# Kernel tuning notes

Hardware: AMD Instinct MI355X
Metric: run time of the kernel (lower is better)

Reference implementation:

```python
import jax, jax.numpy as jnp
import numpy as np
from jax import lax

MID = 64      # mid_size -> token seq len = MID*MID = 4096
DM = 64       # d_model = in_channels
DI = 128      # d_inner = expand * d_model
DS = 16       # d_state
DC = 4        # d_conv
DTR = 4       # dt_rank = ceil(DM/16)
EPS = 1e-5


def conv3x3(x, w):
    return lax.conv_general_dilated(x, w, (1, 1), ((1, 1), (1, 1)),
                                    dimension_numbers=('NCHW', 'OIHW', 'NCHW'))


def layernorm(x, w, b):
    mu = jnp.mean(x, -1, keepdims=True)
    var = jnp.mean((x - mu) ** 2, -1, keepdims=True)
    return (x - mu) * lax.rsqrt(var + EPS) * w + b


def bilinear(x, h, w):
    b, c = x.shape[:2]
    return jax.image.resize(x, (b, c, h, w), method='bilinear', antialias=False)


def mamba(tok, in_w, conv_w, conv_b, xproj_w, dt_w, dt_b, Alog, D, out_w):
    # tok: (b, L, DM)
    b, L, _ = tok.shape
    xz = tok @ in_w.T                                # (b, L, 2*DI)
    xc, z = jnp.split(xz, 2, axis=-1)
    # causal depthwise conv1d over sequence
    xcT = xc.transpose(0, 2, 1)                      # (b, DI, L)
    xconv = lax.conv_general_dilated(xcT, conv_w, (1,), ((DC - 1, 0),),
                                     dimension_numbers=('NCH', 'OIH', 'NCH'),
                                     feature_group_count=DI)
    xconv = xconv + conv_b[None, :, None]
    u = jax.nn.silu(xconv.transpose(0, 2, 1))        # (b, L, DI)
    x_dbl = u @ xproj_w.T                            # (b, L, DTR+2*DS)
    dt, B, C = jnp.split(x_dbl, [DTR, DTR + DS], axis=-1)
    dt = jax.nn.softplus(dt @ dt_w.T + dt_b)         # (b, L, DI)
    A = -jnp.exp(Alog)                               # (DI, DS)
    dA = jnp.exp(dt[..., None] * A)                  # (b, L, DI, DS)
    dBu = dt[..., None] * B[:, :, None, :] * u[..., None]

    def step(h, xs):
        a_t, bu_t = xs
        h = a_t * h + bu_t
        return h, h

    h0 = jnp.zeros((b, DI, DS), dt.dtype)
    _, hs = lax.scan(step, h0, (dA.transpose(1, 0, 2, 3), dBu.transpose(1, 0, 2, 3)))
    y = jnp.einsum('lbns,bls->bln', hs, C) + u * D   # (b, L, DI)
    y = y * jax.nn.silu(z)
    return y @ out_w.T                               # (b, L, DM)


def setup_inputs() -> dict:
    key = jax.random.key(0)
    ks = iter(jax.random.split(key, 32))
    s = 0.02
    d = {}
    d['x'] = jax.random.normal(next(ks), (4, 64, 128, 128), jnp.float32)
    for n, shp in [('cb_w1', (64, 64, 3, 3)), ('cb_w2', (64, 64, 3, 3)),
                   ('sm_w1', (64, 64, 3, 3)), ('sm_w2', (64, 64, 3, 3))]:
        d[n] = jax.random.normal(next(ks), shp, jnp.float32) * s
    d['ln1_w'] = jnp.ones((DM,), jnp.float32); d['ln1_b'] = jnp.zeros((DM,), jnp.float32)
    d['ln2_w'] = jnp.ones((DM,), jnp.float32); d['ln2_b'] = jnp.zeros((DM,), jnp.float32)
    for p in ['m1', 'm2']:
        d[p + '_in_w'] = jax.random.normal(next(ks), (2 * DI, DM), jnp.float32) * s
        d[p + '_conv_w'] = jax.random.normal(next(ks), (DI, 1, DC), jnp.float32) * s
        d[p + '_conv_b'] = jnp.zeros((DI,), jnp.float32)
        d[p + '_xproj_w'] = jax.random.normal(next(ks), (DTR + 2 * DS, DI), jnp.float32) * s
        d[p + '_dt_w'] = jax.random.normal(next(ks), (DI, DTR), jnp.float32) * s
        d[p + '_dt_b'] = jnp.full((DI,), -2.0, jnp.float32)
        d[p + '_Alog'] = jnp.broadcast_to(jnp.log(jnp.arange(1, DS + 1, dtype=jnp.float32)), (DI, DS)).copy()
        d[p + '_D'] = jnp.ones((DI,), jnp.float32)
        d[p + '_out_w'] = jax.random.normal(next(ks), (DM, DI), jnp.float32) * s
    return d


def reference(x, cb_w1, cb_w2, ln1_w, ln1_b, ln2_w, ln2_b,
              m1_in_w, m1_conv_w, m1_conv_b, m1_xproj_w, m1_dt_w, m1_dt_b, m1_Alog, m1_D, m1_out_w,
              m2_in_w, m2_conv_w, m2_conv_b, m2_xproj_w, m2_dt_w, m2_dt_b, m2_Alog, m2_D, m2_out_w,
              sm_w1, sm_w2):
    b, c, h, w = x.shape
    xr = conv3x3(jax.nn.relu(conv3x3(x, cb_w1)), cb_w2) + x
    x_small = xr if (h, w) == (MID, MID) else bilinear(xr, MID, MID)
    tokens = x_small.reshape(b, c, MID * MID).transpose(0, 2, 1)   # (b, L, c)
    main = mamba(layernorm(tokens, ln1_w, ln1_b),
                 m1_in_w, m1_conv_w, m1_conv_b, m1_xproj_w, m1_dt_w, m1_dt_b, m1_Alog, m1_D, m1_out_w)
    gate_feat = mamba(layernorm(tokens, ln2_w, ln2_b),
                      m2_in_w, m2_conv_w, m2_conv_b, m2_xproj_w, m2_dt_w, m2_dt_b, m2_Alog, m2_D, m2_out_w)
    gate = jax.nn.softmax(gate_feat, axis=1)                       # softmax over token dim
    tokens = tokens + gate * main
    feat = tokens.transpose(0, 2, 1).reshape(b, c, MID, MID)
    if (h, w) != (MID, MID):
        feat = bilinear(feat, h, w)
    return conv3x3(jax.nn.relu(conv3x3(feat, sm_w1)), sm_w2)
```

## Files before the change

kernel.cpp:

```cpp
#include <hip/hip_runtime.h>

typedef unsigned int u32;
typedef unsigned short u16;
typedef __attribute__((ext_vector_type(8))) short short8;
typedef __attribute__((ext_vector_type(4))) float f32x4;

__device__ __forceinline__ float sigmoidf_(float x){
  return 1.f / (1.f + __expf(-x));
}
__device__ __forceinline__ u16 f2bf(float f){
  union { float f; u32 i; } v; v.f = f;
  u32 r = v.i + 0x7fffu + ((v.i >> 16) & 1u);
  return (u16)(r >> 16);
}
__device__ __forceinline__ float bf2f(u32 u){
  union { float f; u32 i; } v; v.i = (u & 0xffffu) << 16; return v.f;
}
__device__ __forceinline__ float softplus_(float x){
  return fmaxf(x, 0.f) + __logf(1.f + __expf(-fabsf(x)));
}

__global__ void k_wswz2b(const float* __restrict__ wA, u16* __restrict__ WHA, u16* __restrict__ WLA,
                         const float* __restrict__ wB, u16* __restrict__ WHB, u16* __restrict__ WLB,
                         u16* __restrict__ BPH, u16* __restrict__ BPL){
  int gidx = blockIdx.x * 256 + threadIdx.x;
  if (gidx < 73728){
    int sel = gidx >= 36864;
    int idx = gidx - sel * 36864;
    const float* w = sel ? wB : wA;
    u16* WH = sel ? WHB : WHA;
    u16* WL = sel ? WLB : WLA;
    int j    = idx & 7;
    int lane = (idx >> 3) & 63;
    int nt   = (idx >> 9) & 3;
    int kc   = (idx >> 11) & 1;
    int t    = idx >> 12;
    int ic = kc * 32 + ((lane >> 4) & 3) * 8 + j;
    int oc = nt * 16 + (lane & 15);
    float v = w[(oc * 64 + ic) * 9 + t];
    u16 h = f2bf(v);
    u16 l = f2bf(v - bf2f(h));
    WH[idx] = h; WL[idx] = l;
  } else {
    int i = gidx - 73728;
    if (i >= 2064) return;
    int b = i / 516, p = i - b * 516;
    int y, x;
    if (p < 130){ y = 0; x = p; }
    else if (p < 260){ y = 129; x = p - 130; }
    else if (p < 388){ y = p - 260 + 1; x = 0; }
    else { y = p - 388 + 1; x = 129; }
    size_t o = (((size_t)b * 130 + y) * 130 + x) * 64;
    uint4 z = make_uint4(0, 0, 0, 0);
#pragma unroll
    for (int q = 0; q < 8; q++){
      *(uint4*)(BPH + o + q * 8) = z;
      *(uint4*)(BPL + o + q * 8) = z;
    }
  }
}

__global__ __launch_bounds__(256) void k_prep(const float* __restrict__ src,
                                              u16* __restrict__ PH, u16* __restrict__ PL){
  __shared__ float ld[64 * 129];
  int yp = blockIdx.x;
  int b  = blockIdx.y;
  int ys = yp - 1;
  int tid = threadIdx.x;
  if ((u32)ys < 128u){
    for (int i = tid; i < 8192; i += 256){
      int c = i >> 7, x = i & 127;
      ld[c * 129 + x] = src[((size_t)(b * 64 + c) * 128 + ys) * 128 + x];
    }
  }
  __syncthreads();
  for (int i = tid; i < 130 * 64; i += 256){
    int xp = i >> 6, c = i & 63;
    float v = 0.f;
    if ((u32)ys < 128u && (u32)(xp - 1) < 128u) v = ld[c * 129 + (xp - 1)];
    u16 h = f2bf(v);
    u16 l = f2bf(v - bf2f(h));
    size_t o = (((size_t)b * 130 + yp) * 130 + xp) * 64 + c;
    PH[o] = h; PL[o] = l;
  }
}

__global__ __launch_bounds__(256) void k_prepup(const float* __restrict__ FEAT,
                                                u16* __restrict__ PH, u16* __restrict__ PL){
  __shared__ float ld0[64 * 65], ld1[64 * 65];
  int yp = blockIdx.x;
  int b  = blockIdx.y;
  int ys = yp - 1;
  int tid = threadIdx.x;
  float wy = 0.f;
  if ((u32)ys < 128u){
    float ay = 0.5f * ys - 0.25f;
    int fy = (int)floorf(ay); wy = ay - fy;
    int y0s = fy < 0 ? 0 : fy, y1s = fy + 1 > 63 ? 63 : fy + 1;
    for (int i = tid; i < 1024; i += 256){
      int c = i >> 4, x4 = (i & 15) * 4;
      float4 a0 = *(const float4*)&FEAT[((size_t)(b * 64 + c) * 64 + y0s) * 64 + x4];
      float4 a1 = *(const float4*)&FEAT[((size_t)(b * 64 + c) * 64 + y1s) * 64 + x4];
      ld0[c * 65 + x4 + 0] = a0.x; ld0[c * 65 + x4 + 1] = a0.y;
      ld0[c * 65 + x4 + 2] = a0.z; ld0[c * 65 + x4 + 3] = a0.w;
      ld1[c * 65 + x4 + 0] = a1.x; ld1[c * 65 + x4 + 1] = a1.y;
      ld1[c * 65 + x4 + 2] = a1.z; ld1[c * 65 + x4 + 3] = a1.w;
    }
  }
  __syncthreads();
  for (int i = tid; i < 130 * 64; i += 256){
    int xp = i >> 6, c = i & 63;
    float v = 0.f;
    int xs = xp - 1;
    if ((u32)ys < 128u && (u32)xs < 128u){
      float ax = 0.5f * xs - 0.25f;
      int fx = (int)floorf(ax); float wx = ax - fx;
      int x0s = fx < 0 ? 0 : fx, x1s = fx + 1 > 63 ? 63 : fx + 1;
      float v0 = (1.f - wx) * ld0[c * 65 + x0s] + wx * ld0[c * 65 + x1s];
      float v1 = (1.f - wx) * ld1[c * 65 + x0s] + wx * ld1[c * 65 + x1s];
      v = (1.f - wy) * v0 + wy * v1;
    }
    u16 h = f2bf(v);
    u16 l = f2bf(v - bf2f(h));
    size_t o = (((size_t)b * 130 + yp) * 130 + xp) * 64 + c;
    PH[o] = h; PL[o] = l;
  }
}

__global__ __launch_bounds__(256) void k_convm(
    const u16* __restrict__ PH, const u16* __restrict__ PL,
    const u16* __restrict__ WH, const u16* __restrict__ WL,
    const float* __restrict__ resid,
    u16* __restrict__ OBH, u16* __restrict__ OBL,
    float* __restrict__ OUTF, float* __restrict__ T, float* __restrict__ NT,
    int mode)
{
  __shared__ __align__(16) u32 smem[17344];
  u16* Ah_s = (u16*)smem;
  u16* Al_s = Ah_s + 10368;
  int tid = threadIdx.x;
  int lane = tid & 63, w = tid >> 6;
  int quad = lane >> 4, lcol = lane & 15;
  int b = blockIdx.z, y0 = blockIdx.y * 16, x0 = blockIdx.x * 16;

  f32x4 acc[4][4];
#pragma unroll
  for (int mt = 0; mt < 4; mt++)
#pragma unroll
    for (int nt = 0; nt < 4; nt++)
      acc[mt][nt] = (f32x4){0.f, 0.f, 0.f, 0.f};

  for (int kc = 0; kc < 2; kc++){
    __syncthreads();
    for (int i = tid; i < 1296; i += 256){
      int q = i & 3;
      int rc = i >> 2;
      int r = rc / 18, c = rc - r * 18;
      size_t so = (((size_t)b * 130 + y0 + r) * 130 + (x0 + c)) * 64 + kc * 32 + q * 8;
      int de = rc * 32 + q * 8;
      *(uint4*)(Ah_s + de) = *(const uint4*)(PH + so);
      *(uint4*)(Al_s + de) = *(const uint4*)(PL + so);
    }
    __syncthreads();
#pragma unroll
    for (int t = 0; t < 9; t++){
      int dy = t / 3, dx = t - dy * 3;
      short8 bh[4], bl[4];
#pragma unroll
      for (int nt = 0; nt < 4; nt++){
        int o = ((t * 2 + kc) * 4 + nt) * 512 + lane * 8;
        bh[nt] = *(const short8*)(WH + o);
        bl[nt] = *(const short8*)(WL + o);
      }
      short8 ah[4], al[4];
#pragma unroll
      for (int mt = 0; mt < 4; mt++){
        int e = ((w * 4 + mt + dy) * 18 + (lcol + dx)) * 32 + quad * 8;
        ah[mt] = *(const short8*)(Ah_s + e);
        al[mt] = *(const short8*)(Al_s + e);
      }
#pragma unroll
      for (int mt = 0; mt < 4; mt++)
#pragma unroll
        for (int nt = 0; nt < 4; nt++){
          acc[mt][nt] = __builtin_amdgcn_mfma_f32_16x16x32_bf16(ah[mt], bh[nt], acc[mt][nt], 0, 0, 0);
          acc[mt][nt] = __builtin_amdgcn_mfma_f32_16x16x32_bf16(ah[mt], bl[nt], acc[mt][nt], 0, 0, 0);
          acc[mt][nt] = __builtin_amdgcn_mfma_f32_16x16x32_bf16(al[mt], bh[nt], acc[mt][nt], 0, 0, 0);
        }
    }
  }

  __syncthreads();
  if (mode == 0){
    u32* epi = smem;
#pragma unroll
    for (int mt = 0; mt < 4; mt++){
      int row = w * 4 + mt;
#pragma unroll
      for (int nt = 0; nt < 4; nt++){
#pragma unroll
        for (int reg = 0; reg < 4; reg++){
          float v = fmaxf(acc[mt][nt][reg], 0.f);
          u32 h = f2bf(v);
          u32 l = f2bf(v - bf2f(h));
          int ccol = quad * 4 + reg;
          int oc = nt * 16 + lcol;
          epi[(row * 16 + ccol) * 66 + oc] = h | (l << 16);
        }
      }
    }
    __syncthreads();
    for (int i = tid; i < 16384; i += 256){
      int px = i >> 6, oc = i & 63;
      int row = px >> 4, ccol = px & 15;
      u32 pk = epi[px * 66 + oc];
      size_t o = (((size_t)b * 130 + y0 + row + 1) * 130 + (x0 + ccol + 1)) * 64 + oc;
      OBH[o] = (u16)pk;
      OBL[o] = (u16)(pk >> 16);
    }
  } else {
    float* epi = (float*)smem;
#pragma unroll
    for (int mt = 0; mt < 4; mt++){
      int row = w * 4 + mt;
#pragma unroll
      for (int nt = 0; nt < 4; nt++){
#pragma unroll
        for (int reg = 0; reg < 4; reg++){
          int px = row * 16 + quad * 4 + reg;
          int oc = nt * 16 + lcol;
          epi[oc * 259 + px] = acc[mt][nt][reg];
        }
      }
    }
    __syncthreads();
    if (mode == 1){
      for (int i = tid; i < 16384; i += 256){
        int oc = i >> 8, px = i & 255;
        int row = px >> 4, c = px & 15;
        size_t o = (((size_t)b * 64 + oc) * 128 + y0 + row) * 128 + x0 + c;
        float v = epi[oc * 259 + px];
        if (resid) v += resid[o];
        OUTF[o] = v;
      }
    } else {
      for (int i = tid; i < 16384; i += 256){
        int oc = i >> 8, px = i & 255;
        int row = px >> 4, c = px & 15;
        size_t o = (((size_t)b * 64 + oc) * 128 + y0 + row) * 128 + x0 + c;
        epi[oc * 259 + px] += resid[o];
      }
      __syncthreads();
      float* redS  = (float*)smem + 16576;
      float* redQ  = redS + 320;
      float* stats = redQ + 320;
      int token = tid & 63, cg2 = tid >> 6;
      int tr = token >> 3, tc = token & 7;
      float av[16]; float s = 0.f, q = 0.f;
      int p0 = (2 * tr) * 16 + 2 * tc;
#pragma unroll
      for (int j = 0; j < 16; j++){
        int c = cg2 * 16 + ((j + tr) & 15);
        const float* ep = epi + c * 259;
        float v = 0.25f * (ep[p0] + ep[p0 + 1] + ep[p0 + 16] + ep[p0 + 17]);
        av[j] = v; s += v; q = fmaf(v, v, q);
      }
      redS[token * 5 + cg2] = s;
      redQ[token * 5 + cg2] = q;
      __syncthreads();
      if (tid < 64){
        float S = 0.f, Q = 0.f;
        for (int g = 0; g < 4; g++){ S += redS[tid * 5 + g]; Q += redQ[tid * 5 + g]; }
        float mu = S * (1.f / 64.f);
        float var = Q * (1.f / 64.f) - mu * mu;
        stats[tid * 2] = mu;
        stats[tid * 2 + 1] = rsqrtf(var + 1e-5f);
      }
      __syncthreads();
      float mu = stats[token * 2], inv = stats[token * 2 + 1];
      int l = (blockIdx.y * 8 + tr) * 64 + blockIdx.x * 8 + tc;
      size_t to = ((size_t)b * 4096 + l) * 64;
#pragma unroll
      for (int j = 0; j < 16; j++){
        int c = cg2 * 16 + ((j + tr) & 15);
        T[to + c] = av[j];
        NT[to + c] = (av[j] - mu) * inv;
      }
    }
  }
}

__global__ __launch_bounds__(256) void k_fold2(
    const float* __restrict__ Wa, const float* __restrict__ lnwa, const float* __restrict__ lnba,
    float* __restrict__ W2a, float* __restrict__ B2a,
    const float* __restrict__ Wb, const float* __restrict__ lnwb, const float* __restrict__ lnbb,
    float* __restrict__ W2b, float* __restrict__ B2b){
  int m = blockIdx.x;
  const float* W   = m ? Wb   : Wa;
  const float* lnw = m ? lnwb : lnwa;
  const float* lnb = m ? lnbb : lnba;
  float* W2 = m ? W2b : W2a;
  float* B2 = m ? B2b : B2a;
  __shared__ float gw[64], gb[64];
  int j = threadIdx.x;
  if (j < 64){ gw[j] = lnw[j]; gb[j] = lnb[j]; }
  __syncthreads();
  float bias = 0.f;
#pragma unroll
  for (int k4 = 0; k4 < 16; k4++){
    float4 wv = *(const float4*)&W[j * 64 + k4 * 4];
    W2[j * 64 + k4 * 4 + 0] = wv.x * gw[k4 * 4 + 0];
    W2[j * 64 + k4 * 4 + 1] = wv.y * gw[k4 * 4 + 1];
    W2[j * 64 + k4 * 4 + 2] = wv.z * gw[k4 * 4 + 2];
    W2[j * 64 + k4 * 4 + 3] = wv.w * gw[k4 * 4 + 3];
    bias = fmaf(wv.x, gb[k4 * 4 + 0], bias);
    bias = fmaf(wv.y, gb[k4 * 4 + 1], bias);
    bias = fmaf(wv.z, gb[k4 * 4 + 2], bias);
    bias = fmaf(wv.w, gb[k4 * 4 + 3], bias);
  }
  B2[j] = bias;
}

__global__ __launch_bounds__(256) void k_inprojdw(
    const float* __restrict__ NT,
    const float* __restrict__ W2a, const float* __restrict__ B2a,
    float* __restrict__ Ua, float* __restrict__ Za,
    const float* __restrict__ cwa, const float* __restrict__ cba,
    const float* __restrict__ W2b, const float* __restrict__ B2b,
    float* __restrict__ Ub, float* __restrict__ Zb,
    const float* __restrict__ cwb, const float* __restrict__ cbb)
{
  __shared__ float wL[64 * 68];
  __shared__ float xcs[67 * 68];
  int mz = blockIdx.z;
  const float* W2 = mz ? W2b : W2a;
  const float* B2 = mz ? B2b : B2a;
  float* U = mz ? Ub : Ua;
  float* Z  = mz ? Zb : Za;
  const float* cw = mz ? cwb : cwa;
  const float* cb = mz ? cbb : cba;
  int tid = threadIdx.x;
  int t0 = blockIdx.x * 64;
  int j0 = blockIdx.y * 64;
  for (int i = tid; i < 4096; i += 256){
    int jl = i >> 6, k = i & 63;
    wL[jl * 68 + k] = W2[(size_t)(j0 + jl) * 64 + k];
  }
  __syncthreads();
  int tq = tid >> 4, cg = tid & 15;
  const float* ntp = NT + (size_t)(t0 + tq * 4) * 64;
  float acc[4][4];
#pragma unroll
  for (int c = 0; c < 4; c++){
    float bias = B2[j0 + cg + c * 16];
#pragma unroll
    for (int t = 0; t < 4; t++) acc[t][c] = bias;
  }
#pragma unroll 4
  for (int k4 = 0; k4 < 16; k4++){
    float4 lv[4];
#pragma unroll
    for (int t = 0; t < 4; t++)
      lv[t] = *(const float4*)(ntp + t * 64 + k4 * 4);
    float4 wv[4];
#pragma unroll
    for (int c = 0; c < 4; c++)
      wv[c] = *(const float4*)&wL[(cg + c * 16) * 68 + k4 * 4];
#pragma unroll
    for (int t = 0; t < 4; t++)
#pragma unroll
      for (int c = 0; c < 4; c++){
        acc[t][c] = fmaf(lv[t].x, wv[c].x, acc[t][c]);
        acc[t][c] = fmaf(lv[t].y, wv[c].y, acc[t][c]);
        acc[t][c] = fmaf(lv[t].z, wv[c].z, acc[t][c]);
        acc[t][c] = fmaf(lv[t].w, wv[c].w, acc[t][c]);
      }
  }
  if (j0 < 128){
    int isStart = ((t0 & 4095) == 0);
    if (tid < 192){
      int e = tid >> 6, col = tid & 63;
      float v = 0.f;
      if (!isStart){
        const float* np = NT + (size_t)(t0 - 3 + e) * 64;
        float a2 = B2[j0 + col];
#pragma unroll 4
        for (int k = 0; k < 64; k += 4){
          float4 nv = *(const float4*)(np + k);
          float4 wv = *(const float4*)&wL[col * 68 + k];
          a2 = fmaf(nv.x, wv.x, fmaf(nv.y, wv.y, fmaf(nv.z, wv.z, fmaf(nv.w, wv.w, a2))));
        }
        v = a2;
      }
      xcs[e * 68 + col] = v;
    }
#pragma unroll
    for (int t = 0; t < 4; t++)
#pragma unroll
      for (int c = 0; c < 4; c++)
        xcs[(3 + tq * 4 + t) * 68 + cg + c * 16] = acc[t][c];
    __syncthreads();
#pragma unroll
    for (int c = 0; c < 4; c++){
      int lc = cg + c * 16;
      int ch = j0 + lc;
      float4 wv = *(const float4*)(cw + ch * 4);
      float bias = cb[ch];
#pragma unroll
      for (int t = 0; t < 4; t++){
        int row = 3 + tq * 4 + t;
        float a = bias;
        a = fmaf(wv.w, xcs[row * 68 + lc], a);
        a = fmaf(wv.z, xcs[(row - 1) * 68 + lc], a);
        a = fmaf(wv.y, xcs[(row - 2) * 68 + lc], a);
        a = fmaf(wv.x, xcs[(row - 3) * 68 + lc], a);
        size_t tg = t0 + tq * 4 + t;
        U[tg * 128 + ch] = a * sigmoidf_(a);
      }
    }
  } else {
#pragma unroll
    for (int t = 0; t < 4; t++){
      size_t tg = t0 + tq * 4 + t;
#pragma unroll
      for (int c = 0; c < 4; c++)
        Z[tg * 128 + (j0 - 128) + cg + c * 16] = acc[t][c];
    }
  }
}

__global__ __launch_bounds__(256) void k_xprojdt(
    const float* __restrict__ U0, const float* __restrict__ XW0, float* __restrict__ DBL0,
    const float* __restrict__ U1, const float* __restrict__ XW1, float* __restrict__ DBL1)
{
  __shared__ float xw[36 * 132];
  int bid = blockIdx.x;
  int m = bid >> 7, blk = bid & 127;
  const float* Up   = m ? U1   : U0;
  const float* XWp  = m ? XW1  : XW0;
  float* DBLp = m ? DBL1 : DBL0;
  int tid = threadIdx.x;
  for (int i = tid; i < 4608; i += 256)
    xw[(i >> 7) * 132 + (i & 127)] = XWp[i];
  __syncthreads();
  int slot = tid >> 2, jq = tid & 3;
  size_t tgA = (size_t)blk * 128 + slot;
  size_t tgB = tgA + 64;
  const float4* upA = (const float4*)(Up + tgA * 128);
  const float4* upB = (const float4*)(Up + tgB * 128);
  float accA[9], accB[9];
#pragma unroll
  for (int jj = 0; jj < 9; jj++){ accA[jj] = 0.f; accB[jj] = 0.f; }
  for (int k4 = 0; k4 < 32; k4++){
    float4 uA = upA[k4];
    float4 uB = upB[k4];
#pragma unroll
    for (int jj = 0; jj < 9; jj++){
      float4 w = *(const float4*)&xw[(jq * 9 + jj) * 132 + k4 * 4];
      accA[jj] = fmaf(w.x, uA.x, fmaf(w.y, uA.y, fmaf(w.z, uA.z, fmaf(w.w, uA.w, accA[jj]))));
      accB[jj] = fmaf(w.x, uB.x, fmaf(w.y, uB.y, fmaf(w.z, uB.z, fmaf(w.w, uB.w, accB[jj]))));
    }
  }
#pragma unroll
  for (int jj = 0; jj < 9; jj++){
    DBLp[tgA * 36 + jq * 9 + jj] = accA[jj];
    DBLp[tgB * 36 + jq * 9 + jj] = accB[jj];
  }
}

__global__ __launch_bounds__(256) void k_scanA(
    const float* __restrict__ DBL0, const float* __restrict__ U0, const float* __restrict__ AL0,
    const float* __restrict__ DTW0, const float* __restrict__ DTB0,
    const float* __restrict__ DBL1, const float* __restrict__ U1, const float* __restrict__ AL1,
    const float* __restrict__ DTW1, const float* __restrict__ DTB1,
    float* __restrict__ HF, float* __restrict__ AP)
{
  __shared__ float su[64 * 65], sB[16 * 68], sdtr[256];
  int bid = blockIdx.x;
  int cg = bid & 1;
  int c  = (bid >> 1) & 63;
  int b  = (bid >> 7) & 3;
  int m  = bid >> 9;
  const float* DBLp = m ? DBL1 : DBL0;
  const float* Up   = m ? U1   : U0;
  const float* ALp  = m ? AL1  : AL0;
  const float* DTWp = m ? DTW1 : DTW0;
  const float* DTBp = m ? DTB1 : DTB0;
  int tid = threadIdx.x;
  int lane = tid & 63, w = tid >> 6;
  int lcol = lane & 15, q = lane >> 4;
  int chL = w * 16 + lcol;
  int n = cg * 64 + chL;
  size_t base = (size_t)b * 4096 + c * 64;
  for (int i = tid; i < 4096; i += 256){
    int ch = i & 63, l = i >> 6;
    su[l * 65 + ch] = Up[(base + l) * 128 + cg * 64 + ch];
  }
  for (int i = tid; i < 1024; i += 256){
    int s = i & 15, l = i >> 4;
    sB[s * 68 + l] = DBLp[(base + l) * 36 + 4 + s];
  }
  {
    int l = tid >> 2, jj = tid & 3;
    sdtr[tid] = DBLp[(base + l) * 36 + jj];
  }
  const float LOG2E = 1.4426950408889634f;
  float A1[4];
#pragma unroll
  for (int j = 0; j < 4; j++) A1[j] = -__expf(ALp[n * 16 + q * 4 + j]) * LOG2E;
  float4 wdt = *(const float4*)(DTWp + n * 4);
  float bdt = DTBp[n];
  __syncthreads();
  float h[4] = {0.f, 0.f, 0.f, 0.f};
  float ap[4] = {1.f, 1.f, 1.f, 1.f};
#pragma unroll
  for (int l4 = 0; l4 < 16; l4++){
    float4 Bv[4];
#pragma unroll
    for (int j = 0; j < 4; j++) Bv[j] = *(const float4*)&sB[(q * 4 + j) * 68 + l4 * 4];
#pragma unroll
    for (int jj = 0; jj < 4; jj++){
      int l = l4 * 4 + jj;
      float4 d = *(const float4*)&sdtr[l * 4];
      float x = bdt;
      x = fmaf(wdt.x, d.x, x); x = fmaf(wdt.y, d.y, x);
      x = fmaf(wdt.z, d.z, x); x = fmaf(wdt.w, d.w, x);
      float dt = softplus_(x);
      float u  = su[l * 65 + chL];
      float dtu = dt * u;
#pragma unroll
      for (int j = 0; j < 4; j++){
        float a = exp2f(dt * A1[j]);
        h[j] = fmaf(a, h[j], dtu * (&Bv[j].x)[jj]);
        ap[j] *= a;
      }
    }
  }
  size_t o = ((size_t)((m * 4 + b) * 64 + c)) * 2048 + n * 16 + q * 4;
  *(float4*)&HF[o] = make_float4(h[0], h[1], h[2], h[3]);
  *(float4*)&AP[o] = make_float4(ap[0], ap[1], ap[2], ap[3]);
}

__global__ __launch_bounds__(64) void k_scanB(
    const float* __restrict__ HF, const float* __restrict__ AP, float* __restrict__ HIN)
{
  int r = blockIdx.x * 64 + threadIdx.x;
  int q = r >> 11;
  int p = r & 2047;
  size_t base = (size_t)q * 64 * 2048 + p;
  float h = 0.f;
  for (int c8 = 0; c8 < 8; c8++){
    float a[8], f[8];
#pragma unroll
    for (int j = 0; j < 8; j++){
      size_t o = base + (size_t)(c8 * 8 + j) * 2048;
      a[j] = AP[o]; f[j] = HF[o];
    }
#pragma unroll
    for (int j = 0; j < 8; j++){
      size_t o = base + (size_t)(c8 * 8 + j) * 2048;
      HIN[o] = h;
      h = fmaf(a[j], h, f[j]);
    }
  }
}

__global__ __launch_bounds__(256) void k_scanC(
    const float* __restrict__ DBL0, const float* __restrict__ U0, const float* __restrict__ AL0,
    const float* __restrict__ DTW0, const float* __restrict__ DTB0,
    const float* __restrict__ D0, float* __restrict__ Y0,
    const float* __restrict__ DBL1, const float* __restrict__ U1, const float* __restrict__ AL1,
    const float* __restrict__ DTW1, const float* __restrict__ DTB1,
    const float* __restrict__ D1, float* __restrict__ Y1,
    const float* __restrict__ HIN)
{
  __shared__ float su[64 * 65], sB[16 * 68], sC[16 * 68], sdtr[256];
  int bid = blockIdx.x;
  int cg = bid & 1;
  int c  = (bid >> 1) & 63;
  int b  = (bid >> 7) & 3;
  int m  = bid >> 9;
  const float* DBLp = m ? DBL1 : DBL0;
  const float* Up   = m ? U1   : U0;
  const float* ALp  = m ? AL1  : AL0;
  const float* DTWp = m ? DTW1 : DTW0;
  const float* DTBp = m ? DTB1 : DTB0;
  const float* Dp   = m ? D1   : D0;
  float*       Yp   = m ? Y1   : Y0;
  int tid = threadIdx.x;
  int lane = tid & 63, w = tid >> 6;
  int lcol = lane & 15, q = lane >> 4;
  int chL = w * 16 + lcol;
  int n = cg * 64 + chL;
  size_t base = (size_t)b * 4096 + c * 64;
  for (int i = tid; i < 4096; i += 256){
    int ch = i & 63, l = i >> 6;
    su[l * 65 + ch] = Up[(base + l) * 128 + cg * 64 + ch];
  }
  for (int i = tid; i < 1024; i += 256){
    int s = i & 15, l = i >> 4;
    size_t ob = (base + l) * 36;
    sB[s * 68 + l] = DBLp[ob + 4 + s];
    sC[s * 68 + l] = DBLp[ob + 20 + s];
  }
  {
    int l = tid >> 2, jj = tid & 3;
    sdtr[tid] = DBLp[(base + l) * 36 + jj];
  }
  const float LOG2E = 1.4426950408889634f;
  float A1[4];
#pragma unroll
  for (int j = 0; j < 4; j++) A1[j] = -__expf(ALp[n * 16 + q * 4 + j]) * LOG2E;
  float4 wdt = *(const float4*)(DTWp + n * 4);
  float bdt = DTBp[n];
  float Dn = Dp[n];
  float4 hv = *(const float4*)&HIN[((size_t)((m * 4 + b) * 64 + c)) * 2048 + n * 16 + q * 4];
  float h[4] = {hv.x, hv.y, hv.z, hv.w};
  __syncthreads();
#pragma unroll
  for (int l4 = 0; l4 < 16; l4++){
    float4 Bv[4], Cv[4];
#pragma unroll
    for (int j = 0; j < 4; j++){
      Bv[j] = *(const float4*)&sB[(q * 4 + j) * 68 + l4 * 4];
      Cv[j] = *(const float4*)&sC[(q * 4 + j) * 68 + l4 * 4];
    }
#pragma unroll
    for (int jj = 0; jj < 4; jj++){
      int l = l4 * 4 + jj;
      float4 d = *(const float4*)&sdtr[l * 4];
      float x = bdt;
      x = fmaf(wdt.x, d.x, x); x = fmaf(wdt.y, d.y, x);
      x = fmaf(wdt.z, d.z, x); x = fmaf(wdt.w, d.w, x);
      float dt = softplus_(x);
      float u  = su[l * 65 + chL];
      float dtu = dt * u;
      float p = 0.f;
#pragma unroll
      for (int j = 0; j < 4; j++){
        float a = exp2f(dt * A1[j]);
        h[j] = fmaf(a, h[j], dtu * (&Bv[j].x)[jj]);
        p = fmaf(h[j], (&Cv[j].x)[jj], p);
      }
      p += __shfl_xor(p, 16);
      p += __shfl_xor(p, 32);
      if (q == 0)
        Yp[(base + l) * 128 + n] = fmaf(u, Dn, p);
    }
  }
}

__global__ __launch_bounds__(256) void k_outproj(
    const float* __restrict__ Y0, const float* __restrict__ Zg0,
    const float* __restrict__ W0, float* __restrict__ OUT0,
    const float* __restrict__ Y1, const float* __restrict__ Zg1,
    const float* __restrict__ W1, float* __restrict__ OUT1)
{
  __shared__ float yl[16 * 128];
  __shared__ float wT[128 * 65];
  int m = blockIdx.y;
  const float* Y  = m ? Y1  : Y0;
  const float* Zg = m ? Zg1 : Zg0;
  const float* W  = m ? W1  : W0;
  float* OUT = m ? OUT1 : OUT0;
  int tid = threadIdx.x;
  size_t t0 = (size_t)blockIdx.x * 16;
  for (int i = tid; i < 2048; i += 256){
    float z = Zg[t0 * 128 + i];
    yl[i] = Y[t0 * 128 + i] * (z * sigmoidf_(z));
  }
  for (int i = tid; i < 8192; i += 256){
    int k = i & 127, j = i >> 7;
    wT[k * 65 + j] = W[j * 128 + k];
  }
  __syncthreads();
  int j = tid & 63;
  int tg = tid >> 6;
  float acc[4] = {0.f, 0.f, 0.f, 0.f};
  for (int k = 0; k < 128; k += 4){
    float w0 = wT[k * 65 + j], w1 = wT[(k+1) * 65 + j];
    float w2 = wT[(k+2) * 65 + j], w3 = wT[(k+3) * 65 + j];
#pragma unroll
    for (int t = 0; t < 4; t++){
      float4 yv = *(const float4*)&yl[(tg * 4 + t) * 128 + k];
      acc[t] = fmaf(w0, yv.x, fmaf(w1, yv.y, fmaf(w2, yv.z, fmaf(w3, yv.w, acc[t]))));
    }
  }
#pragma unroll
  for (int t = 0; t < 4; t++)
    OUT[(t0 + tg * 4 + t) * 64 + j] = acc[t];
}

__global__ void k_smA(const float* __restrict__ G, float* __restrict__ P){
  int bid = blockIdx.x;
  int b = bid >> 6, lc = bid & 63;
  int tid = threadIdx.x;
  int j = tid & 63, part = tid >> 6;
  size_t base = (size_t)b * 4096 + lc * 64;
  float mx = -3.4e38f;
  for (int i = 0; i < 16; i++){
    int l = part + i * 4;
    mx = fmaxf(mx, G[(base + l) * 64 + j]);
  }
  float sm = 0.f;
  for (int i = 0; i < 16; i++){
    int l = part + i * 4;
    sm += __expf(G[(base + l) * 64 + j] - mx);
  }
  __shared__ float sM[256], sS[256];
  sM[tid] = mx; sS[tid] = sm;
  __syncthreads();
  if (tid < 64){
    float M = sM[tid], S = sS[tid];
    for (int p = 1; p < 4; p++){
      float m2 = sM[p * 64 + tid], s2 = sS[p * 64 + tid];
      float Mn = fmaxf(M, m2);
      S = S * __expf(M - Mn) + s2 * __expf(m2 - Mn);
      M = Mn;
    }
    P[(bid * 64 + tid) * 2] = M;
    P[(bid * 64 + tid) * 2 + 1] = S;
  }
}

__global__ void k_smB(const float* __restrict__ P, float* __restrict__ F){
  int tid = threadIdx.x;
  int b = tid >> 6, j = tid & 63;
  float M = -3.4e38f, S = 0.f;
  for (int lc = 0; lc < 64; lc++){
    int idx = ((b * 64 + lc) * 64 + j) * 2;
    float m2 = P[idx], s2 = P[idx + 1];
    float Mn = fmaxf(M, m2);
    S = S * __expf(M - Mn) + s2 * __expf(m2 - Mn);
    M = Mn;
  }
  F[(b * 64 + j) * 2] = M;
  F[(b * 64 + j) * 2 + 1] = S;
}

__global__ void k_combine(const float* __restrict__ T, const float* __restrict__ MAIN,
                          const float* __restrict__ G, const float* __restrict__ F,
                          float* __restrict__ FEAT){
  int bid = blockIdx.x;
  int b = bid >> 6, row = bid & 63;
  int tid = threadIdx.x;
  int j = tid & 63, ls = tid >> 6;
  __shared__ float tile[64 * 65];
  float M = F[(b * 64 + j) * 2], invS = 1.f / F[(b * 64 + j) * 2 + 1];
  size_t lbase = (size_t)b * 4096 + row * 64;
  for (int i = 0; i < 16; i++){
    int col = ls + i * 4;
    size_t off = (lbase + col) * 64 + j;
    float g = __expf(G[off] - M) * invS;
    tile[col * 65 + j] = T[off] + g * MAIN[off];
  }
  __syncthreads();
  int colw = tid & 63, jr = tid >> 6;
  for (int jj = jr; jj < 64; jj += 4)
    FEAT[(((size_t)b * 64 + jj) * 64 + row) * 64 + colw] = tile[colw * 65 + jj];
}

extern "C" void kernel_launch(void* const* d_in, const int* in_sizes, int n_in,
                              void* d_out, int out_size, void* d_ws, size_t ws_size,
                              hipStream_t stream) {
  const size_t P1A = 0, P1B = 4326400;
  const size_t MB0 = 0, MB1 = 10027008;
  const size_t O_LN = 0, O_XC = 1048576, O_Z = 3145728, O_U = 5242880,
               O_DBL = 9437184;
  const size_t TOK = 20054016, OUT0 = 21102592, OUT1 = 22151168;
  const size_t FEAT = 23208448;
  const size_t P3A = 4194304, P3B = 8520704;
  const size_t WA_H = 19000000, WA_L = 19018432, WB_H = 19036864, WB_L = 19055296;
  const size_t PADN = 2163200;
  const size_t SMP = 0, SMF = 65536;
  const size_t W2_0 = 21102592, B2_0 = 21118976, W2_1 = 21119232, B2_1 = 21135616;
  const size_t TOTAL = 24257024;
  if (ws_size < TOTAL * 4) return;

  float* ws = (float*)d_ws;
  const float* X   = (const float*)d_in[0];
  const float* CB1 = (const float*)d_in[1];
  const float* CB2 = (const float*)d_in[2];
  const float* SW1 = (const float*)d_in[3];
  const float* SW2 = (const float*)d_in[4];
  const float* LNW[2] = { (const float*)d_in[5], (const float*)d_in[7] };
  const float* LNB[2] = { (const float*)d_in[6], (const float*)d_in[8] };
  const float *INW[2], *CW[2], *CBb[2], *XPW[2], *DTW[2], *DTB[2], *AL[2], *DD[2], *OW[2];
  for (int m = 0; m < 2; m++){
    int p = 9 + m * 9;
    INW[m] = (const float*)d_in[p + 0];
    CW[m]  = (const float*)d_in[p + 1];
    CBb[m] = (const float*)d_in[p + 2];
    XPW[m] = (const float*)d_in[p + 3];
    DTW[m] = (const float*)d_in[p + 4];
    DTB[m] = (const float*)d_in[p + 5];
    AL[m]  = (const float*)d_in[p + 6];
    DD[m]  = (const float*)d_in[p + 7];
    OW[m]  = (const float*)d_in[p + 8];
  }

  u16* wah = (u16*)(ws + WA_H); u16* wal = (u16*)(ws + WA_L);
  u16* wbh = (u16*)(ws + WB_H); u16* wbl = (u16*)(ws + WB_L);

  {
    u16* pah = (u16*)(ws + P1A); u16* pal = pah + PADN * 2;
    u16* pbh = (u16*)(ws + P1B); u16* pbl = pbh + PADN * 2;
    k_wswz2b<<<297, 256, 0, stream>>>(CB1, wah, wal, CB2, wbh, wbl, pbh, pbl);
    k_prep<<<dim3(130, 4), 256, 0, stream>>>(X, pah, pal);
    k_convm<<<dim3(8, 8, 4), 256, 0, stream>>>(pah, pal, wah, wal, nullptr,
                                               pbh, pbl, nullptr, nullptr, nullptr, 0);
    k_convm<<<dim3(8, 8, 4), 256, 0, stream>>>(pbh, pbl, wbh, wbl, X,
                                               nullptr, nullptr, nullptr,
                                               ws + TOK, ws + MB0 + O_LN, 2);
  }

  k_fold2<<<2, 256, 0, stream>>>(INW[0], LNW[0], LNB[0], ws + W2_0, ws + B2_0,
                                 INW[1], LNW[1], LNB[1], ws + W2_1, ws + B2_1);
  k_inprojdw<<<dim3(256, 4, 2), 256, 0, stream>>>(
      ws + MB0 + O_LN,
      ws + W2_0, ws + B2_0, ws + MB0 + O_U, ws + MB0 + O_Z, CW[0], CBb[0],
      ws + W2_1, ws + B2_1, ws + MB1 + O_U, ws + MB1 + O_Z, CW[1], CBb[1]);
  k_xprojdt<<<256, 256, 0, stream>>>(
      ws + MB0 + O_U, XPW[0], ws + MB0 + O_DBL,
      ws + MB1 + O_U, XPW[1], ws + MB1 + O_DBL);

  float* HF  = ws + MB0 + O_XC;
  float* AP  = ws + MB0 + O_XC + 1048576;
  float* HIN = ws + MB0 + O_LN;

  k_scanA<<<1024, 256, 0, stream>>>(
      ws + MB0 + O_DBL, ws + MB0 + O_U, AL[0], DTW[0], DTB[0],
      ws + MB1 + O_DBL, ws + MB1 + O_U, AL[1], DTW[1], DTB[1],
      HF, AP);
  k_scanB<<<256, 64, 0, stream>>>(HF, AP, HIN);
  k_scanC<<<1024, 256, 0, stream>>>(
      ws + MB0 + O_DBL, ws + MB0 + O_U, AL[0], DTW[0], DTB[0], DD[0], ws + MB0 + O_XC,
      ws + MB1 + O_DBL, ws + MB1 + O_U, AL[1], DTW[1], DTB[1], DD[1], ws + MB1 + O_XC,
      HIN);

  k_outproj<<<dim3(1024, 2), 256, 0, stream>>>(
      ws + MB0 + O_XC, ws + MB0 + O_Z, OW[0], ws + OUT0,
      ws + MB1 + O_XC, ws + MB1 + O_Z, OW[1], ws + OUT1);

  k_smA<<<256, 256, 0, stream>>>(ws + OUT1, ws + SMP);
  k_smB<<<1, 256, 0, stream>>>(ws + SMP, ws + SMF);
  k_combine<<<256, 256, 0, stream>>>(ws + TOK, ws + OUT0, ws + OUT1, ws + SMF, ws + FEAT);

  {
    u16* pah = (u16*)(ws + P3A); u16* pal = pah + PADN * 2;
    u16* pbh = (u16*)(ws + P3B); u16* pbl = pbh + PADN * 2;
    k_wswz2b<<<297, 256, 0, stream>>>(SW1, wah, wal, SW2, wbh, wbl, pbh, pbl);
    k_prepup<<<dim3(130, 4), 256, 0, stream>>>(ws + FEAT, pah, pal);
    k_convm<<<dim3(8, 8, 4), 256, 0, stream>>>(pah, pal, wah, wal, nullptr,
                                               pbh, pbl, nullptr, nullptr, nullptr, 0);
    k_convm<<<dim3(8, 8, 4), 256, 0, stream>>>(pbh, pbl, wbh, wbl, nullptr,
                                               nullptr, nullptr, (float*)d_out,
                                               nullptr, nullptr, 1);
  }
}
```

Measured before the change: 397.0 us.

## Restructure chunked selective scan to one channel per thread with 16 states

The chunked scan kernels now give each thread a whole channel with all 16 states in registers, replacing the 4-states-per-lane layout that needed cross-lane shuffles to reduce the C·h output. Chunks shrink from 64 to 32 tokens, which doubles the number of chunks the sequential combine kernel walks. u is read straight from global memory with a two-step register prefetch instead of being staged through shared memory, and only the dt/B/C rows are staged. Scratch buffers move to free workspace regions. In exchange it raises register pressure (16 h, 16 A, 16 ap per thread) and lengthens the serial carry pass.

```diff
diff --git a/kernel.cpp b/kernel.cpp
--- a/kernel.cpp
+++ b/kernel.cpp
@@ -468,77 +468,82 @@
   }
 }
 
-__global__ __launch_bounds__(256) void k_scanA(
+#define STEPA(s, Bel) { float a_ = exp2f(dt * A1[s]); h[s] = fmaf(a_, h[s], dtu * (Bel)); ap[s] *= a_; }
+#define STEPC(s, Bel, Cel) { float a_ = exp2f(dt * A1[s]); h[s] = fmaf(a_, h[s], dtu * (Bel)); p = fmaf(h[s], (Cel), p); }
+
+__global__ __launch_bounds__(128) void k_scanA(
     const float* __restrict__ DBL0, const float* __restrict__ U0, const float* __restrict__ AL0,
     const float* __restrict__ DTW0, const float* __restrict__ DTB0,
     const float* __restrict__ DBL1, const float* __restrict__ U1, const float* __restrict__ AL1,
     const float* __restrict__ DTW1, const float* __restrict__ DTB1,
     float* __restrict__ HF, float* __restrict__ AP)
 {
-  __shared__ float su[64 * 65], sB[16 * 68], sdtr[256];
+  __shared__ float sd[32 * 20];
   int bid = blockIdx.x;
-  int cg = bid & 1;
-  int c  = (bid >> 1) & 63;
-  int b  = (bid >> 7) & 3;
-  int m  = bid >> 9;
+  int c = bid & 127, b = (bid >> 7) & 3, m = bid >> 9;
   const float* DBLp = m ? DBL1 : DBL0;
   const float* Up   = m ? U1   : U0;
   const float* ALp  = m ? AL1  : AL0;
   const float* DTWp = m ? DTW1 : DTW0;
   const float* DTBp = m ? DTB1 : DTB0;
-  int tid = threadIdx.x;
-  int lane = tid & 63, w = tid >> 6;
-  int lcol = lane & 15, q = lane >> 4;
-  int chL = w * 16 + lcol;
-  int n = cg * 64 + chL;
-  size_t base = (size_t)b * 4096 + c * 64;
-  for (int i = tid; i < 4096; i += 256){
-    int ch = i & 63, l = i >> 6;
-    su[l * 65 + ch] = Up[(base + l) * 128 + cg * 64 + ch];
-  }
-  for (int i = tid; i < 1024; i += 256){
-    int s = i & 15, l = i >> 4;
-    sB[s * 68 + l] = DBLp[(base + l) * 36 + 4 + s];
-  }
+  int ch = threadIdx.x;
+  size_t base = (size_t)b * 4096 + c * 32;
+  for (int i = ch; i < 160; i += 128){
+    int l = i / 5, part = i - l * 5;
+    *(float4*)&sd[l * 20 + part * 4] = *(const float4*)&DBLp[(base + l) * 36 + part * 4];
+  }
+  const float LOG2E = 1.4426950408889634f;
+  float A1[16];
   {
-    int l = tid >> 2, jj = tid & 3;
-    sdtr[tid] = DBLp[(base + l) * 36 + jj];
-  }
-  const float LOG2E = 1.4426950408889634f;
-  float A1[4];
-#pragma unroll
-  for (int j = 0; j < 4; j++) A1[j] = -__expf(ALp[n * 16 + q * 4 + j]) * LOG2E;
-  float4 wdt = *(const float4*)(DTWp + n * 4);
-  float bdt = DTBp[n];
-  __syncthreads();
-  float h[4] = {0.f, 0.f, 0.f, 0.f};
-  float ap[4] = {1.f, 1.f, 1.f, 1.f};
-#pragma unroll
-  for (int l4 = 0; l4 < 16; l4++){
-    float4 Bv[4];
-#pragma unroll
-    for (int j = 0; j < 4; j++) Bv[j] = *(const float4*)&sB[(q * 4 + j) * 68 + l4 * 4];
-#pragma unroll
-    for (int jj = 0; jj < 4; jj++){
-      int l = l4 * 4 + jj;
-      float4 d = *(const float4*)&sdtr[l * 4];
-      float x = bdt;
-      x = fmaf(wdt.x, d.x, x); x = fmaf(wdt.y, d.y, x);
-      x = fmaf(wdt.z, d.z, x); x = fmaf(wdt.w, d.w, x);
-      float dt = softplus_(x);
-      float u  = su[l * 65 + chL];
-      float dtu = dt * u;
-#pragma unroll
-      for (int j = 0; j < 4; j++){
-        float a = exp2f(dt * A1[j]);
-        h[j] = fmaf(a, h[j], dtu * (&Bv[j].x)[jj]);
-        ap[j] *= a;
-      }
-    }
-  }
-  size_t o = ((size_t)((m * 4 + b) * 64 + c)) * 2048 + n * 16 + q * 4;
-  *(float4*)&HF[o] = make_float4(h[0], h[1], h[2], h[3]);
-  *(float4*)&AP[o] = make_float4(ap[0], ap[1], ap[2], ap[3]);
+    float4 a0 = *(const float4*)&ALp[ch * 16 + 0];
+    float4 a1 = *(const float4*)&ALp[ch * 16 + 4];
+    float4 a2 = *(const float4*)&ALp[ch * 16 + 8];
+    float4 a3 = *(const float4*)&ALp[ch * 16 + 12];
+    A1[0] = -__expf(a0.x) * LOG2E; A1[1] = -__expf(a0.y) * LOG2E;
+    A1[2] = -__expf(a0.z) * LOG2E; A1[3] = -__expf(a0.w) * LOG2E;
+    A1[4] = -__expf(a1.x) * LOG2E; A1[5] = -__expf(a1.y) * LOG2E;
+    A1[6] = -__expf(a1.z) * LOG2E; A1[7] = -__expf(a1.w) * LOG2E;
+    A1[8] = -__expf(a2.x) * LOG2E; A1[9] = -__expf(a2.y) * LOG2E;
+    A1[10] = -__expf(a2.z) * LOG2E; A1[11] = -__expf(a2.w) * LOG2E;
+    A1[12] = -__expf(a3.x) * LOG2E; A1[13] = -__expf(a3.y) * LOG2E;
+    A1[14] = -__expf(a3.z) * LOG2E; A1[15] = -__expf(a3.w) * LOG2E;
+  }
+  float4 wdt = *(const float4*)(DTWp + ch * 4);
+  float bdt = DTBp[ch];
+  float h[16], ap[16];
+#pragma unroll
+  for (int s = 0; s < 16; s++){ h[s] = 0.f; ap[s] = 1.f; }
+  float ucur = Up[base * 128 + ch];
+  float unx  = Up[(base + 1) * 128 + ch];
+  __syncthreads();
+#pragma unroll
+  for (int l = 0; l < 32; l++){
+    float u2 = (l < 30) ? Up[(base + l + 2) * 128 + ch] : 0.f;
+    float4 d = *(const float4*)&sd[l * 20];
+    float x = bdt;
+    x = fmaf(wdt.x, d.x, x); x = fmaf(wdt.y, d.y, x);
+    x = fmaf(wdt.z, d.z, x); x = fmaf(wdt.w, d.w, x);
+    float dt = softplus_(x);
+    float dtu = dt * ucur;
+    float4 B0 = *(const float4*)&sd[l * 20 + 4];
+    float4 B1 = *(const float4*)&sd[l * 20 + 8];
+    float4 B2 = *(const float4*)&sd[l * 20 + 12];
+    float4 B3 = *(const float4*)&sd[l * 20 + 16];
+    STEPA(0, B0.x) STEPA(1, B0.y) STEPA(2, B0.z) STEPA(3, B0.w)
+    STEPA(4, B1.x) STEPA(5, B1.y) STEPA(6, B1.z) STEPA(7, B1.w)
+    STEPA(8, B2.x) STEPA(9, B2.y) STEPA(10, B2.z) STEPA(11, B2.w)
+    STEPA(12, B3.x) STEPA(13, B3.y) STEPA(14, B3.z) STEPA(15, B3.w)
+    ucur = unx; unx = u2;
+  }
+  size_t o = ((size_t)((m * 4 + b) * 128 + c)) * 2048 + (size_t)ch * 16;
+  *(float4*)&HF[o + 0]  = make_float4(h[0], h[1], h[2], h[3]);
+  *(float4*)&HF[o + 4]  = make_float4(h[4], h[5], h[6], h[7]);
+  *(float4*)&HF[o + 8]  = make_float4(h[8], h[9], h[10], h[11]);
+  *(float4*)&HF[o + 12] = make_float4(h[12], h[13], h[14], h[15]);
+  *(float4*)&AP[o + 0]  = make_float4(ap[0], ap[1], ap[2], ap[3]);
+  *(float4*)&AP[o + 4]  = make_float4(ap[4], ap[5], ap[6], ap[7]);
+  *(float4*)&AP[o + 8]  = make_float4(ap[8], ap[9], ap[10], ap[11]);
+  *(float4*)&AP[o + 12] = make_float4(ap[12], ap[13], ap[14], ap[15]);
 }
 
 __global__ __launch_bounds__(64) void k_scanB(
@@ -547,9 +552,9 @@
   int r = blockIdx.x * 64 + threadIdx.x;
   int q = r >> 11;
   int p = r & 2047;
-  size_t base = (size_t)q * 64 * 2048 + p;
+  size_t base = (size_t)q * 128 * 2048 + p;
   float h = 0.f;
-  for (int c8 = 0; c8 < 8; c8++){
+  for (int c8 = 0; c8 < 16; c8++){
     float a[8], f[8];
 #pragma unroll
     for (int j = 0; j < 8; j++){
@@ -565,7 +570,7 @@
   }
 }
 
-__global__ __launch_bounds__(256) void k_scanC(
+__global__ __launch_bounds__(128) void k_scanC(
     const float* __restrict__ DBL0, const float* __restrict__ U0, const float* __restrict__ AL0,
     const float* __restrict__ DTW0, const float* __restrict__ DTB0,
     const float* __restrict__ D0, float* __restrict__ Y0,
@@ -574,12 +579,9 @@
     const float* __restrict__ D1, float* __restrict__ Y1,
     const float* __restrict__ HIN)
 {
-  __shared__ float su[64 * 65], sB[16 * 68], sC[16 * 68], sdtr[256];
+  __shared__ float sd[32 * 36];
   int bid = blockIdx.x;
-  int cg = bid & 1;
-  int c  = (bid >> 1) & 63;
-  int b  = (bid >> 7) & 3;
-  int m  = bid >> 9;
+  int c = bid & 127, b = (bid >> 7) & 3, m = bid >> 9;
   const float* DBLp = m ? DBL1 : DBL0;
   const float* Up   = m ? U1   : U0;
   const float* ALp  = m ? AL1  : AL0;
@@ -587,66 +589,70 @@
   const float* DTBp = m ? DTB1 : DTB0;
   const float* Dp   = m ? D1   : D0;
   float*       Yp   = m ? Y1   : Y0;
-  int tid = threadIdx.x;
-  int lane = tid & 63, w = tid >> 6;
-  int lcol = lane & 15, q = lane >> 4;
-  int chL = w * 16 + lcol;
-  int n = cg * 64 + chL;
-  size_t base = (size_t)b * 4096 + c * 64;
-  for (int i = tid; i < 4096; i += 256){
-    int ch = i & 63, l = i >> 6;
-    su[l * 65 + ch] = Up[(base + l) * 128 + cg * 64 + ch];
-  }
-  for (int i = tid; i < 1024; i += 256){
-    int s = i & 15, l = i >> 4;
-    size_t ob = (base + l) * 36;
-    sB[s * 68 + l] = DBLp[ob + 4 + s];
-    sC[s * 68 + l] = DBLp[ob + 20 + s];
-  }
+  int ch = threadIdx.x;
+  size_t base = (size_t)b * 4096 + c * 32;
+  for (int i = ch; i < 288; i += 128){
+    int l = i / 9, part = i - l * 9;
+    *(float4*)&sd[l * 36 + part * 4] = *(const float4*)&DBLp[(base + l) * 36 + part * 4];
+  }
+  const float LOG2E = 1.4426950408889634f;
+  float A1[16];
   {
-    int l = tid >> 2, jj = tid & 3;
-    sdtr[tid] = DBLp[(base + l) * 36 + jj];
-  }
-  const float LOG2E = 1.4426950408889634f;
-  float A1[4];
-#pragma unroll
-  for (int j = 0; j < 4; j++) A1[j] = -__expf(ALp[n * 16 + q * 4 + j]) * LOG2E;
-  float4 wdt = *(const float4*)(DTWp + n * 4);
-  float bdt = DTBp[n];
-  float Dn = Dp[n];
-  float4 hv = *(const float4*)&HIN[((size_t)((m * 4 + b) * 64 + c)) * 2048 + n * 16 + q * 4];
-  float h[4] = {hv.x, hv.y, hv.z, hv.w};
-  __syncthreads();
-#pragma unroll
-  for (int l4 = 0; l4 < 16; l4++){
-    float4 Bv[4], Cv[4];
-#pragma unroll
-    for (int j = 0; j < 4; j++){
-      Bv[j] = *(const float4*)&sB[(q * 4 + j) * 68 + l4 * 4];
-      Cv[j] = *(const float4*)&sC[(q * 4 + j) * 68 + l4 * 4];
-    }
-#pragma unroll
-    for (int jj = 0; jj < 4; jj++){
-      int l = l4 * 4 + jj;
-      float4 d = *(const float4*)&sdtr[l * 4];
-      float x = bdt;
-      x = fmaf(wdt.x, d.x, x); x = fmaf(wdt.y, d.y, x);
-      x = fmaf(wdt.z, d.z, x); x = fmaf(wdt.w, d.w, x);
-      float dt = softplus_(x);
-      float u  = su[l * 65 + chL];
-      float dtu = dt * u;
-      float p = 0.f;
-#pragma unroll
-      for (int j = 0; j < 4; j++){
-        float a = exp2f(dt * A1[j]);
-        h[j] = fmaf(a, h[j], dtu * (&Bv[j].x)[jj]);
-        p = fmaf(h[j], (&Cv[j].x)[jj], p);
-      }
-      p += __shfl_xor(p, 16);
-      p += __shfl_xor(p, 32);
-      if (q == 0)
-        Yp[(base + l) * 128 + n] = fmaf(u, Dn, p);
-    }
+    float4 a0 = *(const float4*)&ALp[ch * 16 + 0];
+    float4 a1 = *(const float4*)&ALp[ch * 16 + 4];
+    float4 a2 = *(const float4*)&ALp[ch * 16 + 8];
+    float4 a3 = *(const float4*)&ALp[ch * 16 + 12];
+    A1[0] = -__expf(a0.x) * LOG2E; A1[1] = -__expf(a0.y) * LOG2E;
+    A1[2] = -__expf(a0.z) * LOG2E; A1[3] = -__expf(a0.w) * LOG2E;
+    A1[4] = -__expf(a1.x) * LOG2E; A1[5] = -__expf(a1.y) * LOG2E;
+    A1[6] = -__expf(a1.z) * LOG2E; A1[7] = -__expf(a1.w) * LOG2E;
+    A1[8] = -__expf(a2.x) * LOG2E; A1[9] = -__expf(a2.y) * LOG2E;
+    A1[10] = -__expf(a2.z) * LOG2E; A1[11] = -__expf(a2.w) * LOG2E;
+    A1[12] = -__expf(a3.x) * LOG2E; A1[13] = -__expf(a3.y) * LOG2E;
+    A1[14] = -__expf(a3.z) * LOG2E; A1[15] = -__expf(a3.w) * LOG2E;
+  }
+  float4 wdt = *(const float4*)(DTWp + ch * 4);
+  float bdt = DTBp[ch];
+  float Dn = Dp[ch];
+  float h[16];
+  {
+    size_t o = ((size_t)((m * 4 + b) * 128 + c)) * 2048 + (size_t)ch * 16;
+    float4 h0 = *(const float4*)&HIN[o + 0];
+    float4 h1 = *(const float4*)&HIN[o + 4];
+    float4 h2 = *(const float4*)&HIN[o + 8];
+    float4 h3 = *(const float4*)&HIN[o + 12];
+    h[0] = h0.x; h[1] = h0.y; h[2] = h0.z; h[3] = h0.w;
+    h[4] = h1.x; h[5] = h1.y; h[6] = h1.z; h[7] = h1.w;
+    h[8] = h2.x; h[9] = h2.y; h[10] = h2.z; h[11] = h2.w;
+    h[12] = h3.x; h[13] = h3.y; h[14] = h3.z; h[15] = h3.w;
+  }
+  float ucur = Up[base * 128 + ch];
+  float unx  = Up[(base + 1) * 128 + ch];
+  __syncthreads();
+#pragma unroll
+  for (int l = 0; l < 32; l++){
+    float u2 = (l < 30) ? Up[(base + l + 2) * 128 + ch] : 0.f;
+    float4 d = *(const float4*)&sd[l * 36];
+    float x = bdt;
+    x = fmaf(wdt.x, d.x, x); x = fmaf(wdt.y, d.y, x);
+    x = fmaf(wdt.z, d.z, x); x = fmaf(wdt.w, d.w, x);
+    float dt = softplus_(x);
+    float dtu = dt * ucur;
+    float4 B0 = *(const float4*)&sd[l * 36 + 4];
+    float4 B1 = *(const float4*)&sd[l * 36 + 8];
+    float4 B2 = *(const float4*)&sd[l * 36 + 12];
+    float4 B3 = *(const float4*)&sd[l * 36 + 16];
+    float4 C0 = *(const float4*)&sd[l * 36 + 20];
+    float4 C1 = *(const float4*)&sd[l * 36 + 24];
+    float4 C2 = *(const float4*)&sd[l * 36 + 28];
+    float4 C3 = *(const float4*)&sd[l * 36 + 32];
+    float p = 0.f;
+    STEPC(0, B0.x, C0.x) STEPC(1, B0.y, C0.y) STEPC(2, B0.z, C0.z) STEPC(3, B0.w, C0.w)
+    STEPC(4, B1.x, C1.x) STEPC(5, B1.y, C1.y) STEPC(6, B1.z, C1.z) STEPC(7, B1.w, C1.w)
+    STEPC(8, B2.x, C2.x) STEPC(9, B2.y, C2.y) STEPC(10, B2.z, C2.z) STEPC(11, B2.w, C2.w)
+    STEPC(12, B3.x, C3.x) STEPC(13, B3.y, C3.y) STEPC(14, B3.z, C3.z) STEPC(15, B3.w, C3.w)
+    Yp[(base + l) * 128 + ch] = fmaf(ucur, Dn, p);
+    ucur = unx; unx = u2;
   }
 }
 
@@ -766,7 +772,7 @@
   const size_t P1A = 0, P1B = 4326400;
   const size_t MB0 = 0, MB1 = 10027008;
   const size_t O_LN = 0, O_XC = 1048576, O_Z = 3145728, O_U = 5242880,
-               O_DBL = 9437184;
+               O_SC = 7340032, O_DBL = 9437184;
   const size_t TOK = 20054016, OUT0 = 21102592, OUT1 = 22151168;
   const size_t FEAT = 23208448;
   const size_t P3A = 4194304, P3B = 8520704;
@@ -824,16 +830,16 @@
       ws + MB0 + O_U, XPW[0], ws + MB0 + O_DBL,
       ws + MB1 + O_U, XPW[1], ws + MB1 + O_DBL);
 
-  float* HF  = ws + MB0 + O_XC;
-  float* AP  = ws + MB0 + O_XC + 1048576;
-  float* HIN = ws + MB0 + O_LN;
-
-  k_scanA<<<1024, 256, 0, stream>>>(
+  float* HF  = ws + MB0 + O_SC;
+  float* AP  = ws + MB1 + O_SC;
+  float* HIN = ws + OUT0;
+
+  k_scanA<<<1024, 128, 0, stream>>>(
       ws + MB0 + O_DBL, ws + MB0 + O_U, AL[0], DTW[0], DTB[0],
       ws + MB1 + O_DBL, ws + MB1 + O_U, AL[1], DTW[1], DTB[1],
       HF, AP);
   k_scanB<<<256, 64, 0, stream>>>(HF, AP, HIN);
-  k_scanC<<<1024, 256, 0, stream>>>(
+  k_scanC<<<1024, 128, 0, stream>>>(
       ws + MB0 + O_DBL, ws + MB0 + O_U, AL[0], DTW[0], DTB[0], DD[0], ws + MB0 + O_XC,
       ws + MB1 + O_DBL, ws + MB1 + O_U, AL[1], DTW[1], DTB[1], DD[1], ws + MB1 + O_XC,
       HIN);
```

New measurement: 410.0 us. 3.3% more time.
